# Performance work log

Measured on AMD Instinct MI355X. Metric: run time of the kernel, lower is better.

The kernel has to match this reference:

```python
import jax, jax.numpy as jnp
import numpy as np

B, C, NC, H, W = 8, 128, 19, 128, 256
EPS = 1e-5


def ste_round(x):
    # straight-through-estimator round (Brevitas-style)
    return x + jax.lax.stop_gradient(jnp.round(x) - x)


def quant_weight(w):
    # int4 symmetric per-output-channel fake-quant: levels [-7, 7]
    s = jnp.maximum(jnp.max(jnp.abs(w), axis=(1, 2, 3), keepdims=True) / 7.0, 1e-8)
    wq = jnp.clip(ste_round(w / s), -7.0, 7.0) * s
    return wq, s


def quant_relu(x, s):
    # ReLU + uint4 fake-quant with learned per-tensor scale: levels [0, 15]
    return jnp.clip(ste_round(x / s), 0.0, 15.0) * s


def batchnorm(x, g, b, m, v):
    scale = (g / jnp.sqrt(v + EPS))[None, :, None, None]
    return (x - m[None, :, None, None]) * scale + b[None, :, None, None]


def dwconv3x3(x, w):
    # w: [C,1,3,3], groups=C
    return jax.lax.conv_general_dilated(
        x, w, window_strides=(1, 1), padding=((1, 1), (1, 1)),
        dimension_numbers=('NCHW', 'OIHW', 'NCHW'),
        feature_group_count=x.shape[1])


def pwconv(x, w):
    # 1x1 conv as einsum; w: [O,I,1,1]
    return jnp.einsum('bchw,oc->bohw', x, w[:, :, 0, 0])


def dsconv(x, dw_w, bn1, s1, pw_w, bn2, s2):
    wq, _ = quant_weight(dw_w)
    x = dwconv3x3(x, wq)
    x = batchnorm(x, *bn1)
    x = quant_relu(x, s1)
    wq, _ = quant_weight(pw_w)
    x = pwconv(x, wq)
    x = batchnorm(x, *bn2)
    x = quant_relu(x, s2)
    return x


def setup_inputs() -> dict:
    key = jax.random.key(0)
    ks = jax.random.split(key, 16)
    d = {}
    d['x'] = jax.random.normal(ks[0], (B, C, H, W), dtype=jnp.float32)
    d['dw1_w'] = jax.random.normal(ks[1], (C, 1, 3, 3), dtype=jnp.float32) * 0.1
    d['pw1_w'] = jax.random.normal(ks[2], (C, C, 1, 1), dtype=jnp.float32) * 0.05
    d['dw2_w'] = jax.random.normal(ks[3], (C, 1, 3, 3), dtype=jnp.float32) * 0.1
    d['pw2_w'] = jax.random.normal(ks[4], (C, C, 1, 1), dtype=jnp.float32) * 0.05
    d['cls_w'] = jax.random.normal(ks[5], (NC, C, 1, 1), dtype=jnp.float32) * 0.05
    d['cls_b'] = jax.random.normal(ks[6], (NC,), dtype=jnp.float32) * 0.1
    for i, kk in zip(range(1, 5), ks[7:11]):
        sub = jax.random.split(kk, 4)
        d[f'bn{i}_g'] = 1.0 + 0.1 * jax.random.normal(sub[0], (C,), dtype=jnp.float32)
        d[f'bn{i}_b'] = 0.1 * jax.random.normal(sub[1], (C,), dtype=jnp.float32)
        d[f'bn{i}_m'] = 0.1 * jax.random.normal(sub[2], (C,), dtype=jnp.float32)
        d[f'bn{i}_v'] = jax.random.uniform(sub[3], (C,), dtype=jnp.float32, minval=0.5, maxval=1.5)
    d['s_a1'] = jnp.float32(0.2)
    d['s_a2'] = jnp.float32(0.2)
    d['s_a3'] = jnp.float32(0.2)
    d['s_a4'] = jnp.float32(0.2)
    return d


def reference(x, dw1_w, pw1_w, dw2_w, pw2_w, cls_w, cls_b,
              bn1_g, bn1_b, bn1_m, bn1_v,
              bn2_g, bn2_b, bn2_m, bn2_v,
              bn3_g, bn3_b, bn3_m, bn3_v,
              bn4_g, bn4_b, bn4_m, bn4_v,
              s_a1, s_a2, s_a3, s_a4):
    x = dsconv(x, dw1_w, (bn1_g, bn1_b, bn1_m, bn1_v), s_a1,
               pw1_w, (bn2_g, bn2_b, bn2_m, bn2_v), s_a2)
    x = dsconv(x, dw2_w, (bn3_g, bn3_b, bn3_m, bn3_v), s_a3,
               pw2_w, (bn4_g, bn4_b, bn4_m, bn4_v), s_a4)
    # QuantDropout p=0.1 is identity in eval mode
    wq, sw = quant_weight(cls_w)
    # IntBias: bias quantized with scale = act_scale * weight_scale (per out channel)
    sb = s_a4 * sw[:, 0, 0, 0]
    bq = ste_round(cls_b / sb) * sb
    out = pwconv(x, wq) + bq[None, :, None, None]
    return out
```

## Files before the change

kernel.cpp:

```cpp
#include <hip/hip_runtime.h>

typedef __attribute__((ext_vector_type(4))) float f32x4;
typedef __attribute__((ext_vector_type(8))) short bf16x8;
typedef __attribute__((ext_vector_type(2))) unsigned int u32x2;
typedef __attribute__((ext_vector_type(4))) unsigned int u32x4;

#define EPSV 1e-5f

#define OFF_BUFA 0u
#define OFF_BUFB 33554432u
#define OFF_T    67108864u
#define OFF_WQ1  (OFF_T + 0u)
#define OFF_R3F  (OFF_T + 6144u)
#define OFF_CST3 (OFF_T + 10752u)
#define OFF_CST1 (OFF_T + 12800u)
#define OFF_R2BF (OFF_T + 14848u)
#define OFF_CST2 (OFF_T + 47616u)
#define OFF_R4BF (OFF_T + 49664u)
#define OFF_CST4 (OFF_T + 82432u)
#define OFF_R5BF (OFF_T + 84480u)
#define OFF_CST5 (OFF_T + 92672u)

struct PArgs {
  const float *dw1, *pw1, *dw2, *pw2, *clsw, *clsb;
  const float *g1, *b1, *m1, *v1;
  const float *g2, *b2, *m2, *v2;
  const float *g3, *b3, *m3, *v3;
  const float *g4, *b4, *m4, *v4;
  const float *s1, *s2, *s3, *s4;
};

__device__ __forceinline__ unsigned short f2bf(float f) {
  return (unsigned short)(__builtin_bit_cast(unsigned int, f) >> 16);
}
__device__ __forceinline__ float clip7(float r) { return fminf(fmaxf(r, -7.f), 7.f); }

__device__ __forceinline__ unsigned int qstep(float a, f32x4 c, float s) {
  float t = (a * c.x - c.z) * c.y + c.w;
  float u = t / s;
  float k = fminf(fmaxf(rintf(u), 0.f), 15.f);
  return (unsigned int)k;
}

__device__ __forceinline__ void cvt2(unsigned int d, unsigned int &lo, unsigned int &hi) {
  float f0 = (float)(d & 0xffu);
  float f1 = (float)((d >> 8) & 0xffu);
  float f2 = (float)((d >> 16) & 0xffu);
  float f3 = (float)(d >> 24);
  lo = (__builtin_bit_cast(unsigned int, f0) >> 16) | (__builtin_bit_cast(unsigned int, f1) & 0xffff0000u);
  hi = (__builtin_bit_cast(unsigned int, f2) >> 16) | (__builtin_bit_cast(unsigned int, f3) & 0xffff0000u);
}

__device__ __forceinline__ float wmax16(float v) {
  #pragma unroll
  for (int s = 1; s < 16; s <<= 1) v = fmaxf(v, __shfl_xor(v, s));
  return v;
}
__device__ __forceinline__ float wmax64(float v) {
  #pragma unroll
  for (int s = 1; s < 64; s <<= 1) v = fmaxf(v, __shfl_xor(v, s));
  return v;
}

__global__ __launch_bounds__(64) void prep_kernel(PArgs P, char* __restrict__ ws) {
  int bi = blockIdx.x, l = threadIdx.x;
  float* wq1 = (float*)(ws + OFF_WQ1);
  float* r3f = (float*)(ws + OFF_R3F);
  f32x4* cst1 = (f32x4*)(ws + OFF_CST1);
  f32x4* cst2 = (f32x4*)(ws + OFF_CST2);
  f32x4* cst3 = (f32x4*)(ws + OFF_CST3);
  f32x4* cst4 = (f32x4*)(ws + OFF_CST4);
  unsigned short* r2 = (unsigned short*)(ws + OFF_R2BF);
  unsigned short* r4 = (unsigned short*)(ws + OFF_R4BF);
  unsigned short* r5 = (unsigned short*)(ws + OFF_R5BF);
  float2* cst5 = (float2*)(ws + OFF_CST5);

  if (bi < 128) {
    int c = bi;
    float w = (l < 9) ? P.dw1[c * 9 + l] : 0.f;
    float mx = wmax16(fabsf(w));
    float sq = fmaxf(mx / 7.0f, 1e-8f);
    if (l < 9) wq1[c * 12 + l] = clip7(rintf(w / sq)) * sq;
    if (l == 0) {
      float sc = P.g1[c] / sqrtf(P.v1[c] + EPSV);
      cst1[c] = f32x4{1.f, sc, P.m1[c], P.b1[c]};
    }
  } else if (bi < 256) {
    int o = bi - 128;
    float w0 = P.pw1[o * 128 + l], w1 = P.pw1[o * 128 + 64 + l];
    float mx = wmax64(fmaxf(fabsf(w0), fabsf(w1)));
    float sq = fmaxf(mx / 7.0f, 1e-8f);
    r2[o * 128 + l]      = f2bf(clip7(rintf(w0 / sq)));
    r2[o * 128 + 64 + l] = f2bf(clip7(rintf(w1 / sq)));
    if (l == 0) {
      float sc = P.g2[o] / sqrtf(P.v2[o] + EPSV);
      cst2[o] = f32x4{P.s1[0] * sq, sc, P.m2[o], P.b2[o]};
    }
  } else if (bi < 384) {
    int c = bi - 256;
    float w = (l < 9) ? P.dw2[c * 9 + l] : 0.f;
    float mx = wmax16(fabsf(w));
    float sq = fmaxf(mx / 7.0f, 1e-8f);
    if (l < 9) r3f[l * 128 + c] = clip7(rintf(w / sq));
    if (l == 0) {
      float sc = P.g3[c] / sqrtf(P.v3[c] + EPSV);
      cst3[c] = f32x4{P.s2[0] * sq, sc, P.m3[c], P.b3[c]};
    }
  } else if (bi < 512) {
    int o = bi - 384;
    float w0 = P.pw2[o * 128 + l], w1 = P.pw2[o * 128 + 64 + l];
    float mx = wmax64(fmaxf(fabsf(w0), fabsf(w1)));
    float sq = fmaxf(mx / 7.0f, 1e-8f);
    r4[o * 128 + l]      = f2bf(clip7(rintf(w0 / sq)));
    r4[o * 128 + 64 + l] = f2bf(clip7(rintf(w1 / sq)));
    if (l == 0) {
      float sc = P.g4[o] / sqrtf(P.v4[o] + EPSV);
      cst4[o] = f32x4{P.s3[0] * sq, sc, P.m4[o], P.b4[o]};
    }
  } else {
    int o = bi - 512;
    if (o < 19) {
      float w0 = P.clsw[o * 128 + l], w1 = P.clsw[o * 128 + 64 + l];
      float mx = wmax64(fmaxf(fabsf(w0), fabsf(w1)));
      float sq = fmaxf(mx / 7.0f, 1e-8f);
      r5[o * 128 + l]      = f2bf(clip7(rintf(w0 / sq)));
      r5[o * 128 + 64 + l] = f2bf(clip7(rintf(w1 / sq)));
      if (l == 0) {
        float A5 = P.s4[0] * sq;
        float bq = rintf(P.clsb[o] / A5) * A5;
        cst5[o] = make_float2(A5, bq);
      }
    } else {
      r5[o * 128 + l] = 0; r5[o * 128 + 64 + l] = 0;
      if (l == 0) cst5[o] = make_float2(0.f, 0.f);
    }
  }
}

__global__ __launch_bounds__(512) void dwA_kernel(const float* __restrict__ x,
                                                  char* __restrict__ ws,
                                                  const float* __restrict__ s1p) {
  int bid = blockIdx.x;
  int b = bid & 7, c = bid >> 3;
  int tid = threadIdx.x;
  int wq = tid & 63, wv = tid >> 6;
  int w0 = wq << 2;
  int h0 = wv << 4;
  const float* wp = (const float*)(ws + OFF_WQ1) + c * 12;
  float k0 = wp[0], k1 = wp[1], k2 = wp[2], k3 = wp[3], k4 = wp[4],
        k5 = wp[5], k6 = wp[6], k7 = wp[7], k8 = wp[8];
  f32x4 cs = ((const f32x4*)(ws + OFF_CST1))[c];
  float s_act = *s1p;
  const float* plane = x + (((size_t)((b << 7) | c)) << 15);
  unsigned char* oplane = (unsigned char*)(ws + OFF_BUFB) + (((size_t)((b << 7) | c)) << 15);

  f32x4 vm = {0.f, 0.f, 0.f, 0.f};
  if (h0 > 0) vm = *(const f32x4*)(plane + ((h0 - 1) << 8) + w0);
  f32x4 v0 = *(const f32x4*)(plane + (h0 << 8) + w0);
  f32x4 vp = *(const f32x4*)(plane + ((h0 + 1) << 8) + w0);
  float lm = __shfl_up(vm.w, 1), l0 = __shfl_up(v0.w, 1), lp = __shfl_up(vp.w, 1);
  float rm = __shfl_down(vm.x, 1), r0 = __shfl_down(v0.x, 1), rp = __shfl_down(vp.x, 1);
  if (wq == 0)  { lm = 0.f; l0 = 0.f; lp = 0.f; }
  if (wq == 63) { rm = 0.f; r0 = 0.f; rp = 0.f; }

  #pragma unroll 4
  for (int i = 0; i < 16; i++) {
    int h = h0 + i;
    float y0 = 0.f, y1 = 0.f, y2 = 0.f, y3 = 0.f;
    y0 = fmaf(lm,   k0, y0); y0 = fmaf(vm.x, k1, y0); y0 = fmaf(vm.y, k2, y0);
    y1 = fmaf(vm.x, k0, y1); y1 = fmaf(vm.y, k1, y1); y1 = fmaf(vm.z, k2, y1);
    y2 = fmaf(vm.y, k0, y2); y2 = fmaf(vm.z, k1, y2); y2 = fmaf(vm.w, k2, y2);
    y3 = fmaf(vm.z, k0, y3); y3 = fmaf(vm.w, k1, y3); y3 = fmaf(rm,   k2, y3);

    y0 = fmaf(l0,   k3, y0); y0 = fmaf(v0.x, k4, y0); y0 = fmaf(v0.y, k5, y0);
    y1 = fmaf(v0.x, k3, y1); y1 = fmaf(v0.y, k4, y1); y1 = fmaf(v0.z, k5, y1);
    y2 = fmaf(v0.y, k3, y2); y2 = fmaf(v0.z, k4, y2); y2 = fmaf(v0.w, k5, y2);
    y3 = fmaf(v0.z, k3, y3); y3 = fmaf(v0.w, k4, y3); y3 = fmaf(r0,   k5, y3);

    y0 = fmaf(lp,   k6, y0); y0 = fmaf(vp.x, k7, y0); y0 = fmaf(vp.y, k8, y0);
    y1 = fmaf(vp.x, k6, y1); y1 = fmaf(vp.y, k7, y1); y1 = fmaf(vp.z, k8, y1);
    y2 = fmaf(vp.y, k6, y2); y2 = fmaf(vp.z, k7, y2); y2 = fmaf(vp.w, k8, y2);
    y3 = fmaf(vp.z, k6, y3); y3 = fmaf(vp.w, k7, y3); y3 = fmaf(rp,   k8, y3);

    unsigned int pk = qstep(y0, cs, s_act) | (qstep(y1, cs, s_act) << 8) |
                      (qstep(y2, cs, s_act) << 16) | (qstep(y3, cs, s_act) << 24);
    *(unsigned int*)(oplane + (h << 8) + w0) = pk;

    vm = v0; lm = l0; rm = r0;
    v0 = vp; l0 = lp; r0 = rp;
    f32x4 nv = {0.f, 0.f, 0.f, 0.f};
    if (i < 15 && h + 2 < 128) nv = *(const f32x4*)(plane + ((h + 2) << 8) + w0);
    vp = nv;
    float nl = __shfl_up(nv.w, 1), nr = __shfl_down(nv.x, 1);
    if (wq == 0)  nl = 0.f;
    if (wq == 63) nr = 0.f;
    lp = nl; rp = nr;
  }
}

__global__ __launch_bounds__(256) void tr_kernel(char* __restrict__ ws) {
  __shared__ __align__(16) unsigned char tile[32768];
  int bid = blockIdx.x;
  int b = bid & 7, chunk = bid >> 3;
  int tid = threadIdx.x;
  int pq = tid & 63, cg = tid >> 6;
  int pl0 = pq << 2;
  int sw = (pq & 31) << 2;
  const unsigned char* inb = (const unsigned char*)(ws + OFF_BUFB);
  size_t gp0 = ((size_t)b << 22) + ((size_t)chunk << 8);

  #pragma unroll
  for (int ci = 0; ci < 8; ci++) {
    int c4 = (cg << 5) + (ci << 2);
    unsigned int t0 = *(const unsigned int*)(inb + (((size_t)((b << 7) | (c4 + 0))) << 15) + (chunk << 8) + pl0);
    unsigned int t1 = *(const unsigned int*)(inb + (((size_t)((b << 7) | (c4 + 1))) << 15) + (chunk << 8) + pl0);
    unsigned int t2 = *(const unsigned int*)(inb + (((size_t)((b << 7) | (c4 + 2))) << 15) + (chunk << 8) + pl0);
    unsigned int t3 = *(const unsigned int*)(inb + (((size_t)((b << 7) | (c4 + 3))) << 15) + (chunk << 8) + pl0);
    #pragma unroll
    for (int j = 0; j < 4; j++) {
      unsigned int oj = ((t0 >> (8 * j)) & 0xffu)
                      | (((t1 >> (8 * j)) & 0xffu) << 8)
                      | (((t2 >> (8 * j)) & 0xffu) << 16)
                      | (((t3 >> (8 * j)) & 0xffu) << 24);
      *(unsigned int*)(tile + ((pl0 + j) << 7) + (c4 ^ sw)) = oj;
    }
  }
  __syncthreads();
  unsigned char* gout = (unsigned char*)(ws + OFF_BUFA) + (((size_t)((b << 7) | chunk)) << 15);
  (void)gp0;
  #pragma unroll
  for (int it = 0; it < 8; it++) {
    int idx = (it << 8) + tid;
    int p = idx >> 3, s = idx & 7;
    int px = (p >> 4) & 7, s23 = (p >> 2) & 3;
    u32x4 ch = *(const u32x4*)(tile + (p << 7) + ((s ^ px) << 4));
    unsigned int t0 = ch.x, t1 = ch.y, t2 = ch.z, t3 = ch.w, tt;
    if (s23 & 1) { tt = t0; t0 = t1; t1 = tt; tt = t2; t2 = t3; t3 = tt; }
    if (s23 & 2) { tt = t0; t0 = t2; t2 = tt; tt = t1; t1 = t3; t3 = tt; }
    *(u32x4*)(gout + (idx << 4)) = u32x4{t0, t1, t2, t3};
  }
}

__global__ __launch_bounds__(256) void pw_kernel(const unsigned char* __restrict__ in,
                                                 unsigned char* __restrict__ out,
                                                 const unsigned short* __restrict__ rbf,
                                                 const f32x4* __restrict__ cst,
                                                 const float* __restrict__ sp) {
  __shared__ unsigned char lds[32768];
  int tid = threadIdx.x;
  int p0 = blockIdx.x << 7;
  #pragma unroll
  for (int it = 0; it < 4; it++) {
    int idx = tid + (it << 8);
    int p = idx >> 3, q = idx & 7;
    int kc = q >> 1, lg = (q & 1) << 1, pt = p >> 4;
    u32x4 g = *(const u32x4*)(in + (size_t)(p0 + p) * 128 + q * 16);
    unsigned int a0, a1, a2, a3, a4, a5, a6, a7;
    cvt2(g.x, a0, a1); cvt2(g.y, a2, a3); cvt2(g.z, a4, a5); cvt2(g.w, a6, a7);
    int l1 = (p & 15) | (lg << 4);
    int ad = (((((pt << 2) + kc) << 6) | l1) << 4);
    *(u32x4*)(lds + ad)       = u32x4{a0, a1, a2, a3};
    *(u32x4*)(lds + ad + 256) = u32x4{a4, a5, a6, a7};
  }
  __syncthreads();
  int l = tid & 63, wv = tid >> 6;
  int ob = wv << 5;
  bf16x8 af[2][4];
  #pragma unroll
  for (int ot = 0; ot < 2; ot++)
    #pragma unroll
    for (int kc = 0; kc < 4; kc++) {
      int o = ob + (ot << 4) + (l & 15);
      int k = (kc << 5) + ((l >> 4) << 3);
      af[ot][kc] = *(const bf16x8*)(rbf + o * 128 + k);
    }
  f32x4 acc[2][8];
  #pragma unroll
  for (int ot = 0; ot < 2; ot++)
    #pragma unroll
    for (int pt = 0; pt < 8; pt++) acc[ot][pt] = f32x4{0.f, 0.f, 0.f, 0.f};
  #pragma unroll
  for (int kc = 0; kc < 4; kc++) {
    bf16x8 bb[8];
    #pragma unroll
    for (int pt = 0; pt < 8; pt++)
      bb[pt] = *(const bf16x8*)(lds + ((((((pt << 2) + kc) << 6)) + l) << 4));
    #pragma unroll
    for (int ot = 0; ot < 2; ot++)
      #pragma unroll
      for (int pt = 0; pt < 8; pt++)
        acc[ot][pt] = __builtin_amdgcn_mfma_f32_16x16x32_bf16(af[ot][kc], bb[pt], acc[ot][pt], 0, 0, 0);
  }
  float s_act = *sp;
  #pragma unroll
  for (int ot = 0; ot < 2; ot++) {
    int o0 = ob + (ot << 4) + ((l >> 4) << 2);
    f32x4 c0 = cst[o0], c1 = cst[o0 + 1], c2 = cst[o0 + 2], c3 = cst[o0 + 3];
    #pragma unroll
    for (int pt = 0; pt < 8; pt++) {
      int p = p0 + (pt << 4) + (l & 15);
      f32x4 a = acc[ot][pt];
      unsigned int pk = qstep(a.x, c0, s_act) | (qstep(a.y, c1, s_act) << 8) |
                        (qstep(a.z, c2, s_act) << 16) | (qstep(a.w, c3, s_act) << 24);
      *(unsigned int*)(out + (size_t)p * 128 + o0) = pk;
    }
  }
}

__global__ __launch_bounds__(256) void dw2_kernel(const unsigned char* __restrict__ in,
                                                  unsigned char* __restrict__ out,
                                                  const char* __restrict__ ws,
                                                  const float* __restrict__ sp) {
  __shared__ float tabs[1664];
  const float* src = (const float*)(ws + OFF_R3F);
  for (int i = threadIdx.x; i < 1664; i += 256) tabs[i] = src[i];
  __syncthreads();
  int tid = threadIdx.x;
  int cq = tid & 31, pg = tid >> 5;
  int c4 = cq << 2;
  float wk[9][4];
  #pragma unroll
  for (int t = 0; t < 9; t++) {
    wk[t][0] = tabs[t * 128 + c4];     wk[t][1] = tabs[t * 128 + c4 + 1];
    wk[t][2] = tabs[t * 128 + c4 + 2]; wk[t][3] = tabs[t * 128 + c4 + 3];
  }
  const f32x4* cst3 = (const f32x4*)(tabs + 1152);
  f32x4 cs0 = cst3[c4], cs1 = cst3[c4 + 1], cs2 = cst3[c4 + 2], cs3 = cst3[c4 + 3];
  float s_act = *sp;
  int pbase = (blockIdx.x << 5) + (pg << 2);
  int wbase = pbase & 255, hh = (pbase >> 8) & 127;

  unsigned int xw[3][6];
  #pragma unroll
  for (int r = 0; r < 3; r++) {
    int dh = r - 1;
    bool rowok = (hh + dh >= 0) && (hh + dh <= 127);
    #pragma unroll
    for (int i = 0; i < 6; i++) {
      int wo = wbase + i - 1;
      unsigned int v = 0;
      if (rowok && wo >= 0 && wo <= 255)
        v = *(const unsigned int*)(in + (size_t)(pbase + dh * 256 + (i - 1)) * 128 + c4);
      xw[r][i] = v;
    }
  }
  #pragma unroll
  for (int j = 0; j < 4; j++) {
    float a0 = 0.f, a1 = 0.f, a2 = 0.f, a3 = 0.f;
    #pragma unroll
    for (int r = 0; r < 3; r++) {
      #pragma unroll
      for (int dwi = 0; dwi < 3; dwi++) {
        unsigned int v = xw[r][j + dwi];
        int t = r * 3 + dwi;
        a0 = fmaf((float)(v & 0xffu),         wk[t][0], a0);
        a1 = fmaf((float)((v >> 8) & 0xffu),  wk[t][1], a1);
        a2 = fmaf((float)((v >> 16) & 0xffu), wk[t][2], a2);
        a3 = fmaf((float)(v >> 24),           wk[t][3], a3);
      }
    }
    unsigned int pk = qstep(a0, cs0, s_act) | (qstep(a1, cs1, s_act) << 8) |
                      (qstep(a2, cs2, s_act) << 16) | (qstep(a3, cs3, s_act) << 24);
    *(unsigned int*)(out + (size_t)(pbase + j) * 128 + c4) = pk;
  }
}

__global__ __launch_bounds__(256) void pwcls_kernel(const unsigned char* __restrict__ in,
                                                    float* __restrict__ out,
                                                    const unsigned short* __restrict__ rbf,
                                                    const f32x4* __restrict__ cst,
                                                    const float* __restrict__ sp,
                                                    const unsigned short* __restrict__ r5,
                                                    const float2* __restrict__ cst5) {
  __shared__ unsigned char lds[32768];
  int tid = threadIdx.x;
  int p0 = blockIdx.x << 7;
  #pragma unroll
  for (int it = 0; it < 4; it++) {
    int idx = tid + (it << 8);
    int p = idx >> 3, q = idx & 7;
    int kc = q >> 1, lg = (q & 1) << 1, pt = p >> 4;
    u32x4 g = *(const u32x4*)(in + (size_t)(p0 + p) * 128 + q * 16);
    unsigned int a0, a1, a2, a3, a4, a5, a6, a7;
    cvt2(g.x, a0, a1); cvt2(g.y, a2, a3); cvt2(g.z, a4, a5); cvt2(g.w, a6, a7);
    int l1 = (p & 15) | (lg << 4);
    int ad = (((((pt << 2) + kc) << 6) | l1) << 4);
    *(u32x4*)(lds + ad)       = u32x4{a0, a1, a2, a3};
    *(u32x4*)(lds + ad + 256) = u32x4{a4, a5, a6, a7};
  }
  __syncthreads();
  int l = tid & 63, wv = tid >> 6;
  int ob = wv << 5;
  bf16x8 af[2][4];
  #pragma unroll
  for (int ot = 0; ot < 2; ot++)
    #pragma unroll
    for (int kc = 0; kc < 4; kc++) {
      int o = ob + (ot << 4) + (l & 15);
      int k = (kc << 5) + ((l >> 4) << 3);
      af[ot][kc] = *(const bf16x8*)(rbf + o * 128 + k);
    }
  f32x4 acc[2][8];
  #pragma unroll
  for (int ot = 0; ot < 2; ot++)
    #pragma unroll
    for (int pt = 0; pt < 8; pt++) acc[ot][pt] = f32x4{0.f, 0.f, 0.f, 0.f};
  #pragma unroll
  for (int kc = 0; kc < 4; kc++) {
    bf16x8 bb[8];
    #pragma unroll
    for (int pt = 0; pt < 8; pt++)
      bb[pt] = *(const bf16x8*)(lds + ((((((pt << 2) + kc) << 6)) + l) << 4));
    #pragma unroll
    for (int ot = 0; ot < 2; ot++)
      #pragma unroll
      for (int pt = 0; pt < 8; pt++)
        acc[ot][pt] = __builtin_amdgcn_mfma_f32_16x16x32_bf16(af[ot][kc], bb[pt], acc[ot][pt], 0, 0, 0);
  }
  float s_act = *sp;
  __syncthreads();
  {
    int hsel = (l >> 4) & 1;
    #pragma unroll
    for (int ot = 0; ot < 2; ot++) {
      int o0 = ob + (ot << 4) + ((l >> 4) << 2);
      f32x4 c0 = cst[o0], c1 = cst[o0 + 1], c2 = cst[o0 + 2], c3 = cst[o0 + 3];
      int hi = (ot << 1) + ((l >> 4) >> 1);
      int lfrag = (l & 15) | (hi << 4);
      #pragma unroll
      for (int pt = 0; pt < 8; pt++) {
        f32x4 a = acc[ot][pt];
        unsigned int k0 = qstep(a.x, c0, s_act), k1 = qstep(a.y, c1, s_act);
        unsigned int k2 = qstep(a.z, c2, s_act), k3 = qstep(a.w, c3, s_act);
        unsigned int w0 = (__builtin_bit_cast(unsigned int, (float)k0) >> 16) |
                          (__builtin_bit_cast(unsigned int, (float)k1) & 0xffff0000u);
        unsigned int w1 = (__builtin_bit_cast(unsigned int, (float)k2) >> 16) |
                          (__builtin_bit_cast(unsigned int, (float)k3) & 0xffff0000u);
        int ad = (((((pt << 2) + wv) << 6) | lfrag) << 4) + (hsel << 3);
        *(u32x2*)(lds + ad) = u32x2{w0, w1};
      }
    }
  }
  __syncthreads();
  int pt0 = wv << 1;
  bf16x8 af5[2][4];
  #pragma unroll
  for (int ot = 0; ot < 2; ot++)
    #pragma unroll
    for (int kc = 0; kc < 4; kc++) {
      int o = (ot << 4) + (l & 15);
      int k = (kc << 5) + ((l >> 4) << 3);
      af5[ot][kc] = *(const bf16x8*)(r5 + o * 128 + k);
    }
  f32x4 a5[2][2] = {{{0,0,0,0},{0,0,0,0}},{{0,0,0,0},{0,0,0,0}}};
  #pragma unroll
  for (int kc = 0; kc < 4; kc++) {
    bf16x8 b0 = *(const bf16x8*)(lds + ((((((pt0    ) << 2) + kc) << 6) + l) << 4));
    bf16x8 b1 = *(const bf16x8*)(lds + ((((((pt0 + 1) << 2) + kc) << 6) + l) << 4));
    #pragma unroll
    for (int ot = 0; ot < 2; ot++) {
      a5[ot][0] = __builtin_amdgcn_mfma_f32_16x16x32_bf16(af5[ot][kc], b0, a5[ot][0], 0, 0, 0);
      a5[ot][1] = __builtin_amdgcn_mfma_f32_16x16x32_bf16(af5[ot][kc], b1, a5[ot][1], 0, 0, 0);
    }
  }
  #pragma unroll
  for (int ptl = 0; ptl < 2; ptl++) {
    int p = p0 + ((pt0 + ptl) << 4) + (l & 15);
    int bb = p >> 15, hw = p & 32767;
    float* ob2 = out + (((size_t)bb * 19) << 15) + hw;
    #pragma unroll
    for (int ot = 0; ot < 2; ot++) {
      int obase = (ot << 4) + ((l >> 4) << 2);
      f32x4 a = a5[ot][ptl];
      #pragma unroll
      for (int i = 0; i < 4; i++) {
        int o = obase + i;
        if (o < 19) {
          float2 c5 = cst5[o];
          ob2[(size_t)o << 15] = fmaf(a[i], c5.x, c5.y);
        }
      }
    }
  }
}

extern "C" void kernel_launch(void* const* d_in, const int* in_sizes, int n_in,
                              void* d_out, int out_size, void* d_ws, size_t ws_size,
                              hipStream_t stream) {
  (void)in_sizes; (void)n_in; (void)out_size; (void)ws_size;
  char* ws = (char*)d_ws;
  PArgs P;
  P.dw1  = (const float*)d_in[1];
  P.pw1  = (const float*)d_in[2];
  P.dw2  = (const float*)d_in[3];
  P.pw2  = (const float*)d_in[4];
  P.clsw = (const float*)d_in[5];
  P.clsb = (const float*)d_in[6];
  P.g1 = (const float*)d_in[7];  P.b1 = (const float*)d_in[8];
  P.m1 = (const float*)d_in[9];  P.v1 = (const float*)d_in[10];
  P.g2 = (const float*)d_in[11]; P.b2 = (const float*)d_in[12];
  P.m2 = (const float*)d_in[13]; P.v2 = (const float*)d_in[14];
  P.g3 = (const float*)d_in[15]; P.b3 = (const float*)d_in[16];
  P.m3 = (const float*)d_in[17]; P.v3 = (const float*)d_in[18];
  P.g4 = (const float*)d_in[19]; P.b4 = (const float*)d_in[20];
  P.m4 = (const float*)d_in[21]; P.v4 = (const float*)d_in[22];
  P.s1 = (const float*)d_in[23]; P.s2 = (const float*)d_in[24];
  P.s3 = (const float*)d_in[25]; P.s4 = (const float*)d_in[26];

  const float* x = (const float*)d_in[0];
  unsigned char* bufA = (unsigned char*)(ws + OFF_BUFA);
  unsigned char* bufB = (unsigned char*)(ws + OFF_BUFB);

  prep_kernel<<<544, 64, 0, stream>>>(P, ws);
  dwA_kernel<<<1024, 512, 0, stream>>>(x, ws, P.s1);
  tr_kernel<<<1024, 256, 0, stream>>>(ws);
  pw_kernel<<<2048, 256, 0, stream>>>(bufA, bufB,
      (const unsigned short*)(ws + OFF_R2BF), (const f32x4*)(ws + OFF_CST2), P.s2);
  dw2_kernel<<<8192, 256, 0, stream>>>(bufB, bufA, ws, P.s3);
  pwcls_kernel<<<2048, 256, 0, stream>>>(bufA, (float*)d_out,
      (const unsigned short*)(ws + OFF_R4BF), (const f32x4*)(ws + OFF_CST4), P.s4,
      (const unsigned short*)(ws + OFF_R5BF), (const float2*)(ws + OFF_CST5));
}
```

Measured before the change: 147.9 us.

## Fuse NCHW-to-NHWC transpose into first pointwise conv kernel

Removes the separate transpose kernel. The first pointwise-conv kernel now reads the NCHW uint8 activations directly, transposes bytes in registers, converts them to bf16 and writes them into a swizzled LDS layout for the MFMA operands. The B-operand LDS reads are XOR-swizzled to match. This saves a full round trip of the intermediate tensor through global memory and one kernel launch, at the cost of more ALU byte-shuffling and strided channel loads in the GEMM kernel. Buffer roles for the later kernels are swapped to match.

```diff
diff --git a/kernel.cpp b/kernel.cpp
--- a/kernel.cpp
+++ b/kernel.cpp
@@ -198,69 +198,37 @@
   }
 }
 
-__global__ __launch_bounds__(256) void tr_kernel(char* __restrict__ ws) {
-  __shared__ __align__(16) unsigned char tile[32768];
-  int bid = blockIdx.x;
-  int b = bid & 7, chunk = bid >> 3;
-  int tid = threadIdx.x;
-  int pq = tid & 63, cg = tid >> 6;
-  int pl0 = pq << 2;
-  int sw = (pq & 31) << 2;
-  const unsigned char* inb = (const unsigned char*)(ws + OFF_BUFB);
-  size_t gp0 = ((size_t)b << 22) + ((size_t)chunk << 8);
-
-  #pragma unroll
-  for (int ci = 0; ci < 8; ci++) {
-    int c4 = (cg << 5) + (ci << 2);
-    unsigned int t0 = *(const unsigned int*)(inb + (((size_t)((b << 7) | (c4 + 0))) << 15) + (chunk << 8) + pl0);
-    unsigned int t1 = *(const unsigned int*)(inb + (((size_t)((b << 7) | (c4 + 1))) << 15) + (chunk << 8) + pl0);
-    unsigned int t2 = *(const unsigned int*)(inb + (((size_t)((b << 7) | (c4 + 2))) << 15) + (chunk << 8) + pl0);
-    unsigned int t3 = *(const unsigned int*)(inb + (((size_t)((b << 7) | (c4 + 3))) << 15) + (chunk << 8) + pl0);
-    #pragma unroll
-    for (int j = 0; j < 4; j++) {
-      unsigned int oj = ((t0 >> (8 * j)) & 0xffu)
-                      | (((t1 >> (8 * j)) & 0xffu) << 8)
-                      | (((t2 >> (8 * j)) & 0xffu) << 16)
-                      | (((t3 >> (8 * j)) & 0xffu) << 24);
-      *(unsigned int*)(tile + ((pl0 + j) << 7) + (c4 ^ sw)) = oj;
-    }
-  }
-  __syncthreads();
-  unsigned char* gout = (unsigned char*)(ws + OFF_BUFA) + (((size_t)((b << 7) | chunk)) << 15);
-  (void)gp0;
-  #pragma unroll
-  for (int it = 0; it < 8; it++) {
-    int idx = (it << 8) + tid;
-    int p = idx >> 3, s = idx & 7;
-    int px = (p >> 4) & 7, s23 = (p >> 2) & 3;
-    u32x4 ch = *(const u32x4*)(tile + (p << 7) + ((s ^ px) << 4));
-    unsigned int t0 = ch.x, t1 = ch.y, t2 = ch.z, t3 = ch.w, tt;
-    if (s23 & 1) { tt = t0; t0 = t1; t1 = tt; tt = t2; t2 = t3; t3 = tt; }
-    if (s23 & 2) { tt = t0; t0 = t2; t2 = tt; tt = t1; t1 = t3; t3 = tt; }
-    *(u32x4*)(gout + (idx << 4)) = u32x4{t0, t1, t2, t3};
-  }
-}
-
-__global__ __launch_bounds__(256) void pw_kernel(const unsigned char* __restrict__ in,
-                                                 unsigned char* __restrict__ out,
-                                                 const unsigned short* __restrict__ rbf,
-                                                 const f32x4* __restrict__ cst,
-                                                 const float* __restrict__ sp) {
+__global__ __launch_bounds__(256) void pwn_kernel(const unsigned char* __restrict__ in,
+                                                  unsigned char* __restrict__ out,
+                                                  const unsigned short* __restrict__ rbf,
+                                                  const f32x4* __restrict__ cst,
+                                                  const float* __restrict__ sp) {
   __shared__ unsigned char lds[32768];
   int tid = threadIdx.x;
   int p0 = blockIdx.x << 7;
-  #pragma unroll
-  for (int it = 0; it < 4; it++) {
-    int idx = tid + (it << 8);
-    int p = idx >> 3, q = idx & 7;
-    int kc = q >> 1, lg = (q & 1) << 1, pt = p >> 4;
-    u32x4 g = *(const u32x4*)(in + (size_t)(p0 + p) * 128 + q * 16);
-    unsigned int a0, a1, a2, a3, a4, a5, a6, a7;
-    cvt2(g.x, a0, a1); cvt2(g.y, a2, a3); cvt2(g.z, a4, a5); cvt2(g.w, a6, a7);
-    int l1 = (p & 15) | (lg << 4);
-    int ad = (((((pt << 2) + kc) << 6) | l1) << 4);
-    *(u32x4*)(lds + ad)       = u32x4{a0, a1, a2, a3};
-    *(u32x4*)(lds + ad + 256) = u32x4{a4, a5, a6, a7};
+  int b_img = p0 >> 15, loc0 = p0 & 32767;
+  {
+    int pb = tid & 7, cq = tid >> 3;
+    int c4 = cq << 2;
+    int kc = cq >> 3, lgr = (cq >> 1) & 3, half = cq & 1;
+    const unsigned char* ib = in + (((size_t)(b_img << 7)) << 15) + loc0 + (pb << 4);
+    u32x4 t0 = *(const u32x4*)(ib + ((size_t)(c4 + 0) << 15));
+    u32x4 t1 = *(const u32x4*)(ib + ((size_t)(c4 + 1) << 15));
+    u32x4 t2 = *(const u32x4*)(ib + ((size_t)(c4 + 2) << 15));
+    u32x4 t3 = *(const u32x4*)(ib + ((size_t)(c4 + 3) << 15));
+    int swz = (pb & 7) << 4;
+    #pragma unroll
+    for (int s = 0; s < 16; s++) {
+      int wrd = s >> 2, sh8 = (s & 3) << 3;
+      unsigned int chw = ((t0[wrd] >> sh8) & 0xffu)
+                       | (((t1[wrd] >> sh8) & 0xffu) << 8)
+                       | (((t2[wrd] >> sh8) & 0xffu) << 16)
+                       | (((t3[wrd] >> sh8) & 0xffu) << 24);
+      unsigned int lo, hi;
+      cvt2(chw, lo, hi);
+      int ad = ((((((pb << 2) + kc) << 6) | s | (lgr << 4)) << 4) + (half << 3)) ^ swz;
+      *(u32x2*)(lds + ad) = u32x2{lo, hi};
+    }
   }
   __syncthreads();
   int l = tid & 63, wv = tid >> 6;
@@ -284,7 +252,7 @@
     bf16x8 bb[8];
     #pragma unroll
     for (int pt = 0; pt < 8; pt++)
-      bb[pt] = *(const bf16x8*)(lds + ((((((pt << 2) + kc) << 6)) + l) << 4));
+      bb[pt] = *(const bf16x8*)(lds + (((((((pt << 2) + kc) << 6)) + l) << 4) ^ ((pt & 7) << 4)));
     #pragma unroll
     for (int ot = 0; ot < 2; ot++)
       #pragma unroll
@@ -513,11 +481,10 @@
 
   prep_kernel<<<544, 64, 0, stream>>>(P, ws);
   dwA_kernel<<<1024, 512, 0, stream>>>(x, ws, P.s1);
-  tr_kernel<<<1024, 256, 0, stream>>>(ws);
-  pw_kernel<<<2048, 256, 0, stream>>>(bufA, bufB,
+  pwn_kernel<<<2048, 256, 0, stream>>>(bufB, bufA,
       (const unsigned short*)(ws + OFF_R2BF), (const f32x4*)(ws + OFF_CST2), P.s2);
-  dw2_kernel<<<8192, 256, 0, stream>>>(bufB, bufA, ws, P.s3);
-  pwcls_kernel<<<2048, 256, 0, stream>>>(bufA, (float*)d_out,
+  dw2_kernel<<<8192, 256, 0, stream>>>(bufA, bufB, ws, P.s3);
+  pwcls_kernel<<<2048, 256, 0, stream>>>(bufB, (float*)d_out,
       (const unsigned short*)(ws + OFF_R4BF), (const f32x4*)(ws + OFF_CST4), P.s4,
       (const unsigned short*)(ws + OFF_R5BF), (const float2*)(ws + OFF_CST5));
 }
```

Result: faster. 136.4 us (-7.8%).
